# Optimization experiments

Measured on AMD Instinct MI355X. Metric: run time of the kernel, lower is better.

The kernel has to match this reference:

```python
import jax, jax.numpy as jnp
import numpy as np

N_MLP = 1024  # number of independent tiny MLPs
D_IN, D_HID, D_OUT = 2, 4, 1
B = 16384


def setup_inputs() -> dict:
    key = jax.random.key(0)
    k = jax.random.split(key, 6)
    x = jax.random.normal(k[0], (B, N_MLP), dtype=jnp.float32)
    x_aug = jax.random.normal(k[1], (B, N_MLP), dtype=jnp.float32)
    # Stacked per-MLP parameters (nn.Linear default init ~ U(-1/sqrt(fan_in), 1/sqrt(fan_in)))
    s1 = 1.0 / np.sqrt(D_IN)
    s2 = 1.0 / np.sqrt(D_HID)
    W1 = jax.random.uniform(k[2], (N_MLP, D_HID, D_IN), jnp.float32, -s1, s1)
    b1 = jax.random.uniform(k[3], (N_MLP, D_HID), jnp.float32, -s1, s1)
    W2 = jax.random.uniform(k[4], (N_MLP, D_OUT, D_HID), jnp.float32, -s2, s2)
    b2 = jax.random.uniform(k[5], (N_MLP, D_OUT), jnp.float32, -s2, s2)
    return {"x": x, "x_aug": x_aug, "W1": W1, "b1": b1, "W2": W2, "b2": b2}


def reference(x, x_aug, W1, b1, W2, b2):
    # data: [B, N, 2] — pair (original, augmented) per feature
    data = jnp.stack([x, x_aug], axis=-1)
    # batched tiny GEMM across the N_MLP axis: [B,N,2] x [N,4,2] -> [B,N,4]
    h = jax.nn.relu(jnp.einsum('bne,nhe->bnh', data, W1) + b1)
    # [B,N,4] x [N,1,4] -> [B,N,1]
    o = jnp.einsum('bnh,noh->bno', h, W2) + b2
    # concat over dim1 of per-MLP [B,1] outputs == squeeze -> [B,N]; mean over N -> [B]
    return jnp.mean(o[..., 0], axis=1)
```

## Files before the change

kernel.cpp:

```cpp
#include <hip/hip_runtime.h>


constexpr int N_MLP = 1024;
constexpr int BATCH = 16384;
constexpr int ROWS = 16;
constexpr int NTHREADS = 256;
constexpr int QN = 256;
constexpr int NQ = N_MLP / QN;

typedef __attribute__((address_space(3))) void lds_void;
typedef const __attribute__((address_space(1))) void gbl_void;

__global__ __launch_bounds__(256)
void zero_out_kernel(float* __restrict__ out) {
    out[blockIdx.x * 256 + threadIdx.x] = 0.0f;
}

__global__ __launch_bounds__(NTHREADS)
void disc_mlp_kernel(const float* __restrict__ x,
                     const float* __restrict__ xa,
                     const float* __restrict__ W1,
                     const float* __restrict__ b1,
                     const float* __restrict__ W2,
                     const float* __restrict__ b2,
                     float* __restrict__ out)
{
    __shared__ float xbuf[ROWS * QN];
    __shared__ float abuf[ROWS * QN];
    __shared__ float red[NTHREADS / 64][ROWS];

    const int t    = threadIdx.x;
    const int lane = t & 63;
    const int wave = t >> 6;
    const int q  = blockIdx.x & (NQ - 1);
    const int rb = blockIdx.x >> 2;
    const int b0 = rb * ROWS;
    const int n  = q * QN + t;

    const float4 p0 = reinterpret_cast<const float4*>(W1)[(size_t)n * 2];
    const float4 p1 = reinterpret_cast<const float4*>(W1)[(size_t)n * 2 + 1];
    const float4 bb = reinterpret_cast<const float4*>(b1)[n];
    const float4 ww = reinterpret_cast<const float4*>(W2)[n];
    const float  b2r = b2[n];

    const float* gx = x  + (size_t)b0 * N_MLP + q * QN;
    const float* ga = xa + (size_t)b0 * N_MLP + q * QN;
#pragma unroll
    for (int i = 0; i < ROWS / 4; ++i) {
        const int r = wave * (ROWS / 4) + i;
        const float* srcx = gx + (size_t)r * N_MLP + lane * 4;
        const float* srca = ga + (size_t)r * N_MLP + lane * 4;
        __builtin_amdgcn_global_load_lds((gbl_void*)srcx,
                                         (lds_void*)&xbuf[r * QN + lane * 4],
                                         16, 0, 0);
        __builtin_amdgcn_global_load_lds((gbl_void*)srca,
                                         (lds_void*)&abuf[r * QN + lane * 4],
                                         16, 0, 0);
    }
    __syncthreads();

    const float A[4]   = {p0.x, p0.z, p1.x, p1.z};
    const float C[4]   = {p0.y, p0.w, p1.y, p1.w};
    const float B1r[4] = {bb.x, bb.y, bb.z, bb.w};
    const float V[4]   = {ww.x, ww.y, ww.z, ww.w};

    float acc[ROWS];
#pragma unroll
    for (int r = 0; r < ROWS; ++r) {
        const float xe  = xbuf[r * QN + t];
        const float xae = abuf[r * QN + t];
        float s = b2r;
#pragma unroll
        for (int j = 0; j < 4; ++j) {
            float h = fmaf(A[j], xe, fmaf(C[j], xae, B1r[j]));
            h = fmaxf(h, 0.0f);
            s = fmaf(V[j], h, s);
        }
        acc[r] = s;
    }

#pragma unroll
    for (int r = 0; r < ROWS; ++r) {
        float v = acc[r];
        v += __shfl_down(v, 32);
        v += __shfl_down(v, 16);
        v += __shfl_down(v, 8);
        v += __shfl_down(v, 4);
        v += __shfl_down(v, 2);
        v += __shfl_down(v, 1);
        if (lane == 0) red[wave][r] = v;
    }
    __syncthreads();
    if (t < ROWS) {
        float s = (red[0][t] + red[1][t]) + (red[2][t] + red[3][t]);
        atomicAdd(out + b0 + t, s * (1.0f / (float)N_MLP));
    }
}

extern "C" void kernel_launch(void* const* d_in, const int* in_sizes, int n_in,
                              void* d_out, int out_size, void* d_ws, size_t ws_size,
                              hipStream_t stream) {
    const float* x  = (const float*)d_in[0];
    const float* xa = (const float*)d_in[1];
    const float* W1 = (const float*)d_in[2];
    const float* b1 = (const float*)d_in[3];
    const float* W2 = (const float*)d_in[4];
    const float* b2 = (const float*)d_in[5];
    float* out = (float*)d_out;

    zero_out_kernel<<<BATCH / 256, 256, 0, stream>>>(out);
    disc_mlp_kernel<<<(BATCH / ROWS) * NQ, NTHREADS, 0, stream>>>(x, xa, W1, b1, W2, b2, out);
}
```

Measured before the change: 150.9 us.

## Give each block full MLP width, drop atomics and zero-init kernel

Each block now covers all 1024 MLPs for 8 rows, with every thread handling 4 adjacent MLPs through float4 loads straight from global memory instead of staging through LDS with global_load_lds. Because a block owns whole rows, the row sum is written directly, which removes the atomicAdd and the separate zero-out launch. The reduction goes through an LDS transpose followed by wave shuffles. Each thread now holds 4 MLPs' parameters in registers, which raises register pressure, and the occupancy hint is set to 4.

```diff
diff --git a/kernel.cpp b/kernel.cpp
--- a/kernel.cpp
+++ b/kernel.cpp
@@ -3,20 +3,10 @@
 
 constexpr int N_MLP = 1024;
 constexpr int BATCH = 16384;
-constexpr int ROWS = 16;
+constexpr int ROWS = 8;
 constexpr int NTHREADS = 256;
-constexpr int QN = 256;
-constexpr int NQ = N_MLP / QN;
 
-typedef __attribute__((address_space(3))) void lds_void;
-typedef const __attribute__((address_space(1))) void gbl_void;
-
-__global__ __launch_bounds__(256)
-void zero_out_kernel(float* __restrict__ out) {
-    out[blockIdx.x * 256 + threadIdx.x] = 0.0f;
-}
-
-__global__ __launch_bounds__(NTHREADS)
+__global__ __launch_bounds__(NTHREADS, 4)
 void disc_mlp_kernel(const float* __restrict__ x,
                      const float* __restrict__ xa,
                      const float* __restrict__ W1,
@@ -25,75 +15,71 @@
                      const float* __restrict__ b2,
                      float* __restrict__ out)
 {
-    __shared__ float xbuf[ROWS * QN];
-    __shared__ float abuf[ROWS * QN];
-    __shared__ float red[NTHREADS / 64][ROWS];
+    __shared__ float red[ROWS][NTHREADS];
 
     const int t    = threadIdx.x;
     const int lane = t & 63;
     const int wave = t >> 6;
-    const int q  = blockIdx.x & (NQ - 1);
-    const int rb = blockIdx.x >> 2;
-    const int b0 = rb * ROWS;
-    const int n  = q * QN + t;
+    const int b0   = blockIdx.x * ROWS;
+    const int m0   = t * 4;
 
-    const float4 p0 = reinterpret_cast<const float4*>(W1)[(size_t)n * 2];
-    const float4 p1 = reinterpret_cast<const float4*>(W1)[(size_t)n * 2 + 1];
-    const float4 bb = reinterpret_cast<const float4*>(b1)[n];
-    const float4 ww = reinterpret_cast<const float4*>(W2)[n];
-    const float  b2r = b2[n];
+    float4 q0[4], q1[4], bv[4], wv[4];
+#pragma unroll
+    for (int m = 0; m < 4; ++m) {
+        q0[m] = reinterpret_cast<const float4*>(W1)[(size_t)(m0 + m) * 2];
+        q1[m] = reinterpret_cast<const float4*>(W1)[(size_t)(m0 + m) * 2 + 1];
+        bv[m] = reinterpret_cast<const float4*>(b1)[m0 + m];
+        wv[m] = reinterpret_cast<const float4*>(W2)[m0 + m];
+    }
+    const float4 b2v = reinterpret_cast<const float4*>(b2)[t];
+    const float bsum = (b2v.x + b2v.y) + (b2v.z + b2v.w);
 
-    const float* gx = x  + (size_t)b0 * N_MLP + q * QN;
-    const float* ga = xa + (size_t)b0 * N_MLP + q * QN;
-#pragma unroll
-    for (int i = 0; i < ROWS / 4; ++i) {
-        const int r = wave * (ROWS / 4) + i;
-        const float* srcx = gx + (size_t)r * N_MLP + lane * 4;
-        const float* srca = ga + (size_t)r * N_MLP + lane * 4;
-        __builtin_amdgcn_global_load_lds((gbl_void*)srcx,
-                                         (lds_void*)&xbuf[r * QN + lane * 4],
-                                         16, 0, 0);
-        __builtin_amdgcn_global_load_lds((gbl_void*)srca,
-                                         (lds_void*)&abuf[r * QN + lane * 4],
-                                         16, 0, 0);
-    }
-    __syncthreads();
-
-    const float A[4]   = {p0.x, p0.z, p1.x, p1.z};
-    const float C[4]   = {p0.y, p0.w, p1.y, p1.w};
-    const float B1r[4] = {bb.x, bb.y, bb.z, bb.w};
-    const float V[4]   = {ww.x, ww.y, ww.z, ww.w};
+    const float4* xp = reinterpret_cast<const float4*>(x  + (size_t)b0 * N_MLP) + t;
+    const float4* ap = reinterpret_cast<const float4*>(xa + (size_t)b0 * N_MLP) + t;
+    constexpr int STRIDE4 = N_MLP / 4;
 
     float acc[ROWS];
 #pragma unroll
     for (int r = 0; r < ROWS; ++r) {
-        const float xe  = xbuf[r * QN + t];
-        const float xae = abuf[r * QN + t];
-        float s = b2r;
+        const float4 xv = xp[r * STRIDE4];
+        const float4 av = ap[r * STRIDE4];
+        const float xe[4] = {xv.x, xv.y, xv.z, xv.w};
+        const float ae[4] = {av.x, av.y, av.z, av.w};
+        float s = bsum;
 #pragma unroll
-        for (int j = 0; j < 4; ++j) {
-            float h = fmaf(A[j], xe, fmaf(C[j], xae, B1r[j]));
-            h = fmaxf(h, 0.0f);
-            s = fmaf(V[j], h, s);
+        for (int m = 0; m < 4; ++m) {
+            float h0 = fmaf(q0[m].x, xe[m], fmaf(q0[m].y, ae[m], bv[m].x));
+            float h1 = fmaf(q0[m].z, xe[m], fmaf(q0[m].w, ae[m], bv[m].y));
+            float h2 = fmaf(q1[m].x, xe[m], fmaf(q1[m].y, ae[m], bv[m].z));
+            float h3 = fmaf(q1[m].z, xe[m], fmaf(q1[m].w, ae[m], bv[m].w));
+            h0 = fmaxf(h0, 0.0f);
+            h1 = fmaxf(h1, 0.0f);
+            h2 = fmaxf(h2, 0.0f);
+            h3 = fmaxf(h3, 0.0f);
+            s = fmaf(wv[m].x, h0, s);
+            s = fmaf(wv[m].y, h1, s);
+            s = fmaf(wv[m].z, h2, s);
+            s = fmaf(wv[m].w, h3, s);
         }
         acc[r] = s;
     }
 
 #pragma unroll
-    for (int r = 0; r < ROWS; ++r) {
-        float v = acc[r];
+    for (int r = 0; r < ROWS; ++r) red[r][t] = acc[r];
+    __syncthreads();
+
+#pragma unroll
+    for (int k = 0; k < ROWS / 4; ++k) {
+        const int r = wave * (ROWS / 4) + k;
+        float v = (red[r][lane] + red[r][lane + 64]) +
+                  (red[r][lane + 128] + red[r][lane + 192]);
         v += __shfl_down(v, 32);
         v += __shfl_down(v, 16);
         v += __shfl_down(v, 8);
         v += __shfl_down(v, 4);
         v += __shfl_down(v, 2);
         v += __shfl_down(v, 1);
-        if (lane == 0) red[wave][r] = v;
-    }
-    __syncthreads();
-    if (t < ROWS) {
-        float s = (red[0][t] + red[1][t]) + (red[2][t] + red[3][t]);
-        atomicAdd(out + b0 + t, s * (1.0f / (float)N_MLP));
+        if (lane == 0) out[b0 + r] = v * (1.0f / (float)N_MLP);
     }
 }
 
@@ -108,6 +94,5 @@
     const float* b2 = (const float*)d_in[5];
     float* out = (float*)d_out;
 
-    zero_out_kernel<<<BATCH / 256, 256, 0, stream>>>(out);
-    disc_mlp_kernel<<<(BATCH / ROWS) * NQ, NTHREADS, 0, stream>>>(x, xa, W1, b1, W2, b2, out);
+    disc_mlp_kernel<<<BATCH / ROWS, NTHREADS, 0, stream>>>(x, xa, W1, b1, W2, b2, out);
 }
```

New measurement: 157.6 us. +4.4%, slower.
